# Performance work log

Measured on AMD Instinct MI355X. Metric: run time of the kernel, lower is better.

Reference implementation:

```python
import jax, jax.numpy as jnp
import numpy as np

N_NODES = 50000
N_EDGES = 50000  # hyperedges
NNZ = 500000
N_GRAPHS = 50
IN_C, HID, OUT_C = 128, 256, 2


def _inv_deg(idx, num_segments):
    deg = jax.ops.segment_sum(jnp.ones(idx.shape[0], jnp.float32), idx, num_segments=num_segments)
    return jnp.where(deg > 0, 1.0 / deg, 0.0)


def hg_conv(x, W, b, rows, cols, dinv, binv):
    # PyG HypergraphConv (no attention, unit edge weights):
    # X' = D^{-1} H B^{-1} H^T (X Theta) + bias
    x = x @ W                                                    # [N, hid]
    e = jax.ops.segment_sum(x[rows], cols, num_segments=N_EDGES) * binv[:, None]   # edge feats [E, hid]
    out = jax.ops.segment_sum(e[cols], rows, num_segments=N_NODES) * dinv[:, None]  # node feats [N, hid]
    return out + b


def setup_inputs() -> dict:
    key = jax.random.key(0)
    ks = jax.random.split(key, 12)
    x = jax.random.normal(ks[0], (N_NODES, IN_C), jnp.float32)
    edge_index = jax.random.randint(ks[1], (2, NNZ), 0, N_EDGES, dtype=jnp.int64)
    batch = jnp.sort(jax.random.randint(ks[2], (N_NODES,), 0, N_GRAPHS, dtype=jnp.int64))
    s = 0.05
    return {
        "x": x, "edge_index": edge_index, "batch": batch,
        "W0": jax.random.normal(ks[3], (IN_C, HID), jnp.float32) * s,
        "b0": jnp.zeros((HID,), jnp.float32),
        "W1": jax.random.normal(ks[4], (HID, HID), jnp.float32) * s,
        "b1": jnp.zeros((HID,), jnp.float32),
        "W2": jax.random.normal(ks[5], (HID, HID), jnp.float32) * s,
        "b2": jnp.zeros((HID,), jnp.float32),
        "M1": jax.random.normal(ks[6], (HID, HID), jnp.float32) * s,
        "bM1": jnp.zeros((HID,), jnp.float32),
        "M2": jax.random.normal(ks[7], (HID, OUT_C), jnp.float32) * s,
        "bM2": jnp.zeros((OUT_C,), jnp.float32),
    }


def reference(x, edge_index, batch, W0, b0, W1, b1, W2, b2, M1, bM1, M2, bM2):
    rows, cols = edge_index[0], edge_index[1]
    dinv = _inv_deg(rows, N_NODES)   # node degree inverse
    binv = _inv_deg(cols, N_EDGES)   # hyperedge degree inverse
    h = jax.nn.relu(hg_conv(x, W0, b0, rows, cols, dinv, binv))
    h = jax.nn.relu(hg_conv(h, W1, b1, rows, cols, dinv, binv))
    h = jax.nn.relu(hg_conv(h, W2, b2, rows, cols, dinv, binv))
    # global_mean_pool (dropout is identity in eval mode)
    cnt = jax.ops.segment_sum(jnp.ones(N_NODES, jnp.float32), batch, num_segments=N_GRAPHS)
    pooled = jax.ops.segment_sum(h, batch, num_segments=N_GRAPHS) / jnp.maximum(cnt, 1.0)[:, None]
    # MLP head
    out = jax.nn.relu(pooled @ M1 + bM1) @ M2 + bM2
    return out
```

## Files before the change

### kernel.cpp

```cpp
#include <hip/hip_runtime.h>
#include <hip/hip_bf16.h>

#define NN   50000
#define NE   50000
#define NNZV 500000
#define NG   50
#define INC  128
#define HID  256
#define OUTC 2
#define STRIDE 32

typedef __bf16 bf16_t;
typedef __bf16 bf16x8 __attribute__((ext_vector_type(8)));
typedef float  f32x4  __attribute__((ext_vector_type(4)));
typedef float  f32x2  __attribute__((ext_vector_type(2)));

__device__ __forceinline__ bf16_t f2b(float f) {
  union { __hip_bfloat16 h; bf16_t b; } u;
  u.h = __float2bfloat16(f);
  return u.b;
}
__device__ __forceinline__ float b2f(bf16_t b) { return (float)b; }

template <bool HI>
__device__ __forceinline__ unsigned int fp8_pk2(float a, float b, unsigned int old) {
  return __builtin_amdgcn_cvt_pk_fp8_f32(a, b, old, HI);
}
__device__ __forceinline__ uint4 fp8_pk16(const float* v) {
  uint4 o;
  unsigned int* ow = &o.x;
#pragma unroll
  for (int wd = 0; wd < 4; wd++) {
    unsigned int u = fp8_pk2<false>(v[wd * 4 + 0], v[wd * 4 + 1], 0u);
    ow[wd] = fp8_pk2<true>(v[wd * 4 + 2], v[wd * 4 + 3], u);
  }
  return o;
}
__device__ __forceinline__ void fp8_acc16(uint4 v, f32x2* a2) {
  a2[0] += __builtin_amdgcn_cvt_pk_f32_fp8(v.x, false);
  a2[1] += __builtin_amdgcn_cvt_pk_f32_fp8(v.x, true);
  a2[2] += __builtin_amdgcn_cvt_pk_f32_fp8(v.y, false);
  a2[3] += __builtin_amdgcn_cvt_pk_f32_fp8(v.y, true);
  a2[4] += __builtin_amdgcn_cvt_pk_f32_fp8(v.z, false);
  a2[5] += __builtin_amdgcn_cvt_pk_f32_fp8(v.z, true);
  a2[6] += __builtin_amdgcn_cvt_pk_f32_fp8(v.w, false);
  a2[7] += __builtin_amdgcn_cvt_pk_f32_fp8(v.w, true);
}

__device__ __forceinline__ void wswiz_one(const float* __restrict__ W, bf16_t* __restrict__ wsw, int t) {
  int lane = t & 63;
  int nt   = (t >> 6) & 15;
  int kc   = t >> 10;
  int q = lane >> 4, n16 = lane & 15;
  bf16x8 o;
#pragma unroll
  for (int j = 0; j < 8; j++)
    o[j] = f2b(W[(size_t)(kc * 32 + q * 8 + j) * HID + nt * 16 + n16]);
  reinterpret_cast<bf16x8*>(wsw)[t] = o;
}

#define FILL_EPT   4
#define FILL_CHUNK (256 * FILL_EPT)
#define FILL_B     ((NNZV + FILL_CHUNK - 1) / FILL_CHUNK)
#define PREP_BX 1563
#define PREP_BW 80
#define PREP_BG 196

__global__ void build_kernel(const int* __restrict__ rows, const int* __restrict__ cols,
                             int* __restrict__ ncur, int* __restrict__ ecur,
                             unsigned short* __restrict__ ncol, unsigned short* __restrict__ erow,
                             const float* __restrict__ x, unsigned char* __restrict__ xb8,
                             const float* __restrict__ W0, const float* __restrict__ W1,
                             const float* __restrict__ W2, bf16_t* __restrict__ w0,
                             bf16_t* __restrict__ w1, bf16_t* __restrict__ w2,
                             const int* __restrict__ batch, int* __restrict__ gstart) {
  int blk = blockIdx.x;
  if (blk < 2 * FILL_B) {
    const bool nodeside = blk >= FILL_B;
    int local = nodeside ? blk - FILL_B : blk;
    int base  = local * FILL_CHUNK + threadIdx.x;
    int key[FILL_EPT], val[FILL_EPT], slot[FILL_EPT];
    bool ok[FILL_EPT];
#pragma unroll
    for (int e = 0; e < FILL_EPT; e++) {
      int i  = base + e * 256;
      ok[e]  = (i < NNZV);
      int ii = ok[e] ? i : 0;
      int r = rows[ii], c = cols[ii];
      key[e] = nodeside ? r : c;
      val[e] = nodeside ? c : r;
    }
    int* cur             = nodeside ? ncur : ecur;
    unsigned short* lstd = nodeside ? ncol : erow;
#pragma unroll
    for (int e = 0; e < FILL_EPT; e++)
      if (ok[e]) slot[e] = atomicAdd(&cur[key[e]], 1);
#pragma unroll
    for (int e = 0; e < FILL_EPT; e++)
      if (ok[e] && slot[e] < STRIDE)
        lstd[((size_t)key[e] << 5) + slot[e]] = (unsigned short)val[e];
  } else if (blk < 2 * FILL_B + PREP_BX) {
    int t = (blk - 2 * FILL_B) * 256 + threadIdx.x;
    if (t >= NN * INC / 16) return;
    const f32x4* p = reinterpret_cast<const f32x4*>(x) + (size_t)t * 4;
    float v[16];
#pragma unroll
    for (int wd = 0; wd < 4; wd++) {
      f32x4 q4 = p[wd];
#pragma unroll
      for (int j = 0; j < 4; j++) v[wd * 4 + j] = q4[j];
    }
    reinterpret_cast<uint4*>(xb8)[t] = fp8_pk16(v);
  } else if (blk < 2 * FILL_B + PREP_BX + PREP_BW) {
    int t = (blk - 2 * FILL_B - PREP_BX) * 256 + threadIdx.x;
    const int C0 = (INC / 32) * 1024;
    const int C1 = (HID / 32) * 1024;
    if (t < C0)                wswiz_one(W0, w0, t);
    else if (t < C0 + C1)      wswiz_one(W1, w1, t - C0);
    else if (t < C0 + 2 * C1)  wswiz_one(W2, w2, t - C0 - C1);
  } else {
    int i = (blk - 2 * FILL_B - PREP_BX - PREP_BW) * 256 + threadIdx.x;
    if (i >= NN) return;
    int cur  = batch[i];
    int prev = (i == 0) ? -1 : batch[i - 1];
    for (int g = prev + 1; g <= cur; g++) gstart[g] = i;
    if (i == NN - 1) {
      for (int g = cur + 1; g <= NG; g++) gstart[g] = NN;
    }
  }
}

template <int K>
__device__ __forceinline__ void gather_direct(const unsigned char* __restrict__ src,
                                              const int* __restrict__ cnt,
                                              const unsigned short* __restrict__ lst,
                                              int seg, int lr, float* acc, int& c) {
  constexpr int LPR = K / 16;
  c = min(cnt[seg], STRIDE);
  const unsigned short* p = lst + ((size_t)seg << 5);
  const uint4* sv = reinterpret_cast<const uint4*>(src);
  f32x2* a2 = reinterpret_cast<f32x2*>(acc);
#pragma unroll
  for (int k = 0; k < 8; k++) a2[k] = f32x2{0.f, 0.f};
  for (int i0 = 0; i0 < c; i0 += 8) {
    int m = c - i0;
    uint4 v[8];
#pragma unroll
    for (int j = 0; j < 8; j++)
      if (j < m) v[j] = sv[(size_t)p[i0 + j] * LPR + lr];
#pragma unroll
    for (int j = 0; j < 8; j++)
      if (j < m) fp8_acc16(v[j], a2);
  }
}

template <int W>
__global__ __launch_bounds__(256) void seg_gather_kernel(const unsigned char* __restrict__ src,
                                                         const int* __restrict__ cnt,
                                                         const unsigned short* __restrict__ lst,
                                                         unsigned char* __restrict__ dst, int nseg) {
  constexpr int LPR = W / 16;
  constexpr int SPW = 64 / LPR;
  constexpr int SPB = 4 * SPW;
  const int lane = threadIdx.x & 63;
  const int wid  = threadIdx.x >> 6;
  const int sub  = lane / LPR, lr = lane % LPR;
  int seg = blockIdx.x * SPB + wid * SPW + sub;
  if (seg >= nseg) return;
  float acc[16];
  int c;
  gather_direct<W>(src, cnt, lst, seg, lr, acc, c);
  float sc = (c > 0) ? (1.0f / (float)c) : 0.f;
  float v16[16];
#pragma unroll
  for (int k = 0; k < 16; k++) v16[k] = acc[k] * sc;
  reinterpret_cast<uint4*>(dst + (size_t)seg * W + lr * 16)[0] = fp8_pk16(v16);
}

template <int K, bool GRELU, bool EPI, bool OUT8>
__global__ __launch_bounds__(256) void ngemm_kernel(const unsigned char* __restrict__ src,
                                                    const int* __restrict__ cnt,
                                                    const unsigned short* __restrict__ lst,
                                                    const float* __restrict__ gbias,
                                                    const bf16_t* __restrict__ wsw,
                                                    const float* __restrict__ ebias,
                                                    void* __restrict__ Bout, int M) {
  constexpr int SW = K + 8;
  __shared__ bf16_t arows[16 * SW];
  const int tid  = threadIdx.x;
  const int wid  = tid >> 6;
  const int lane = tid & 63;
  const int mblk = blockIdx.x * 16;

  constexpr int LPR = K / 16;
  constexpr int SPW = 64 / LPR;
  const int sub = lane / LPR, lr = lane % LPR;
  {
    int row = wid * SPW + sub;
    int seg = mblk + row;
    if (seg < M) {
      float acc[16];
      int c;
      gather_direct<K>(src, cnt, lst, seg, lr, acc, c);
      float sc = (c > 0) ? (1.0f / (float)c) : 0.f;
      bf16_t* dp = arows + row * SW + lr * 16;
      bf16x8 o0, o1;
#pragma unroll
      for (int k = 0; k < 8; k++) {
        float v0 = acc[k] * sc, v1 = acc[k + 8] * sc;
        if constexpr (GRELU) {
          v0 = fmaxf(v0 + gbias[lr * 16 + k], 0.f);
          v1 = fmaxf(v1 + gbias[lr * 16 + k + 8], 0.f);
        }
        o0[k] = f2b(v0);
        o1[k] = f2b(v1);
      }
      reinterpret_cast<bf16x8*>(dp)[0] = o0;
      reinterpret_cast<bf16x8*>(dp)[1] = o1;
    }
  }
  __syncthreads();

  const int q = lane >> 4, n16 = lane & 15;
  f32x4 acc2[4];
#pragma unroll
  for (int j = 0; j < 4; j++) acc2[j] = f32x4{0.f, 0.f, 0.f, 0.f};

  const bf16x8* wv = reinterpret_cast<const bf16x8*>(wsw);
  for (int kc = 0; kc < K / 32; kc++) {
    bf16x8 af = *reinterpret_cast<const bf16x8*>(arows + n16 * SW + kc * 32 + q * 8);
    const bf16x8* wp = wv + (size_t)kc * 1024 + (size_t)(wid * 4) * 64 + lane;
#pragma unroll
    for (int j = 0; j < 4; j++) {
      bf16x8 bf = wp[j * 64];
      acc2[j] = __builtin_amdgcn_mfma_f32_16x16x32_bf16(af, bf, acc2[j], 0, 0, 0);
    }
  }

  float bcol[4];
  if constexpr (EPI) {
#pragma unroll
    for (int j = 0; j < 4; j++) bcol[j] = ebias[(wid * 4 + j) * 16 + n16];
  }

  int mb = mblk + q * 4;
#pragma unroll
  for (int r = 0; r < 4; r++) {
    int m = mb + r;
    if (m < M) {
      if constexpr (OUT8) {
        unsigned char* dst = (unsigned char*)Bout + (size_t)m * HID + n16;
#pragma unroll
        for (int j = 0; j < 4; j++) {
          float v = acc2[j][r];
          if constexpr (EPI) v = fmaxf(v + bcol[j], 0.f);
          unsigned int wbits = fp8_pk2<false>(v, v, 0u);
          dst[(wid * 4 + j) << 4] = (unsigned char)(wbits & 0xffu);
        }
      } else {
        bf16_t* dst = (bf16_t*)Bout + (size_t)m * HID + n16;
#pragma unroll
        for (int j = 0; j < 4; j++) {
          float v = acc2[j][r];
          if constexpr (EPI) v = fmaxf(v + bcol[j], 0.f);
          dst[(wid * 4 + j) << 4] = f2b(v);
        }
      }
    }
  }
}

template <int K>
__global__ __launch_bounds__(256) void ngemm2_kernel(const unsigned char* __restrict__ src,
                                                     const int* __restrict__ cnt,
                                                     const unsigned short* __restrict__ lst,
                                                     const bf16_t* __restrict__ wswA,
                                                     const float* __restrict__ biasA,
                                                     const bf16_t* __restrict__ wswB,
                                                     unsigned char* __restrict__ Bout, int M) {
  constexpr int SW  = K + 8;
  constexpr int SW2 = HID + 8;
  constexpr int LPR = K / 16;
  constexpr int SPW = 64 / LPR;
  __shared__ bf16_t arows[32 * SW];
  __shared__ bf16_t brows[32 * SW2];
  const int tid  = threadIdx.x;
  const int wid  = tid >> 6;
  const int lane = tid & 63;
  const int mblk = blockIdx.x * 32;

  {
    const int sub = lane / LPR, lr = lane % LPR;
    int row = wid * SPW + sub;
    int seg = mblk + row;
    if (seg < M) {
      float acc[16];
      int c;
      gather_direct<K>(src, cnt, lst, seg, lr, acc, c);
      float sc = (c > 0) ? (1.0f / (float)c) : 0.f;
      bf16_t* dp = arows + row * SW + lr * 16;
      bf16x8 o0, o1;
#pragma unroll
      for (int k = 0; k < 8; k++) {
        o0[k] = f2b(acc[k] * sc);
        o1[k] = f2b(acc[k + 8] * sc);
      }
      reinterpret_cast<bf16x8*>(dp)[0] = o0;
      reinterpret_cast<bf16x8*>(dp)[1] = o1;
    }
  }
  __syncthreads();

  const int q = lane >> 4, n16 = lane & 15;
  {
    f32x4 acc2[2][4];
#pragma unroll
    for (int a = 0; a < 2; a++)
#pragma unroll
      for (int j = 0; j < 4; j++) acc2[a][j] = f32x4{0.f, 0.f, 0.f, 0.f};
    const bf16x8* wv = reinterpret_cast<const bf16x8*>(wswA);
    for (int kc = 0; kc < K / 32; kc++) {
      bf16x8 af0 = *reinterpret_cast<const bf16x8*>(arows + n16 * SW + kc * 32 + q * 8);
      bf16x8 af1 = *reinterpret_cast<const bf16x8*>(arows + (n16 + 16) * SW + kc * 32 + q * 8);
      const bf16x8* wp = wv + (size_t)kc * 1024 + (size_t)(wid * 4) * 64 + lane;
#pragma unroll
      for (int j = 0; j < 4; j++) {
        bf16x8 bf = wp[j * 64];
        acc2[0][j] = __builtin_amdgcn_mfma_f32_16x16x32_bf16(af0, bf, acc2[0][j], 0, 0, 0);
        acc2[1][j] = __builtin_amdgcn_mfma_f32_16x16x32_bf16(af1, bf, acc2[1][j], 0, 0, 0);
      }
    }
#pragma unroll
    for (int a = 0; a < 2; a++) {
#pragma unroll
      for (int j = 0; j < 4; j++) {
        float bj = biasA[(wid * 4 + j) * 16 + n16];
#pragma unroll
        for (int r = 0; r < 4; r++) {
          float v = fmaxf(acc2[a][j][r] + bj, 0.f);
          brows[(a * 16 + q * 4 + r) * SW2 + (wid * 4 + j) * 16 + n16] = f2b(v);
        }
      }
    }
  }
  __syncthreads();

  f32x4 acc3[2][4];
#pragma unroll
  for (int a = 0; a < 2; a++)
#pragma unroll
    for (int j = 0; j < 4; j++) acc3[a][j] = f32x4{0.f, 0.f, 0.f, 0.f};
  const bf16x8* wv = reinterpret_cast<const bf16x8*>(wswB);
  for (int kc = 0; kc < HID / 32; kc++) {
    bf16x8 af0 = *reinterpret_cast<const bf16x8*>(brows + n16 * SW2 + kc * 32 + q * 8);
    bf16x8 af1 = *reinterpret_cast<const bf16x8*>(brows + (n16 + 16) * SW2 + kc * 32 + q * 8);
    const bf16x8* wp = wv + (size_t)kc * 1024 + (size_t)(wid * 4) * 64 + lane;
#pragma unroll
    for (int j = 0; j < 4; j++) {
      bf16x8 bf = wp[j * 64];
      acc3[0][j] = __builtin_amdgcn_mfma_f32_16x16x32_bf16(af0, bf, acc3[0][j], 0, 0, 0);
      acc3[1][j] = __builtin_amdgcn_mfma_f32_16x16x32_bf16(af1, bf, acc3[1][j], 0, 0, 0);
    }
  }

#pragma unroll
  for (int a = 0; a < 2; a++) {
    int mb = mblk + a * 16 + q * 4;
#pragma unroll
    for (int r = 0; r < 4; r++) {
      int m = mb + r;
      if (m < M) {
        unsigned char* dst = Bout + (size_t)m * HID + n16;
#pragma unroll
        for (int j = 0; j < 4; j++) {
          float v = acc3[a][j][r];
          unsigned int wbits = fp8_pk2<false>(v, v, 0u);
          dst[(wid * 4 + j) << 4] = (unsigned char)(wbits & 0xffu);
        }
      }
    }
  }
}

__global__ __launch_bounds__(256) void npool_kernel(const unsigned char* __restrict__ src,
                                                    const int* __restrict__ cnt,
                                                    const unsigned short* __restrict__ lst,
                                                    const float* __restrict__ bias,
                                                    const int* __restrict__ batch,
                                                    float* __restrict__ pooled) {
  constexpr int K = HID, SW = K + 8;
  __shared__ bf16_t arows[16 * SW];
  const int tid  = threadIdx.x;
  const int wid  = tid >> 6;
  const int lane = tid & 63;
  const int mblk = blockIdx.x * 16;

  constexpr int LPR = K / 16;
  constexpr int SPW = 64 / LPR;
  const int sub = lane / LPR, lr = lane % LPR;
  {
    int row = wid * SPW + sub;
    int seg = mblk + row;
    if (seg < NN) {
      float acc[16];
      int c;
      gather_direct<K>(src, cnt, lst, seg, lr, acc, c);
      float sc = (c > 0) ? (1.0f / (float)c) : 0.f;
      bf16_t* dp = arows + row * SW + lr * 16;
      bf16x8 o0, o1;
#pragma unroll
      for (int k = 0; k < 8; k++) {
        o0[k] = f2b(fmaxf(acc[k] * sc + bias[lr * 16 + k], 0.f));
        o1[k] = f2b(fmaxf(acc[k + 8] * sc + bias[lr * 16 + k + 8], 0.f));
      }
      reinterpret_cast<bf16x8*>(dp)[0] = o0;
      reinterpret_cast<bf16x8*>(dp)[1] = o1;
    }
  }
  __syncthreads();

  int f = tid;
  float acc = 0.f;
  int curg = -1;
  for (int r = 0; r < 16; r++) {
    int node = mblk + r;
    if (node >= NN) break;
    int g = batch[node];
    if (g != curg) {
      if (curg >= 0) atomicAdd(&pooled[(size_t)curg * HID + f], acc);
      curg = g; acc = 0.f;
    }
    acc += b2f(arows[r * SW + f]);
  }
  if (curg >= 0) atomicAdd(&pooled[(size_t)curg * HID + f], acc);
}

__global__ void head_kernel(const float* __restrict__ pooled, const int* __restrict__ gstart,
                            const float* __restrict__ M1, const float* __restrict__ bM1,
                            const float* __restrict__ M2, const float* __restrict__ bM2,
                            float* __restrict__ out) {
  int g = blockIdx.x;
  int t = threadIdx.x;
  __shared__ float p[HID];
  __shared__ float red[256];
  float cntf = (float)(gstart[g + 1] - gstart[g]);
  float inv = 1.f / fmaxf(cntf, 1.f);
  p[t] = pooled[(size_t)g * HID + t] * inv;
  __syncthreads();
  float h = bM1[t];
  for (int k = 0; k < HID; k++) h += p[k] * M1[k * HID + t];
  h = fmaxf(h, 0.f);
  float c0 = h * M2[t * OUTC + 0];
  float c1 = h * M2[t * OUTC + 1];
  red[t] = c0;
  __syncthreads();
  for (int off = 128; off > 0; off >>= 1) {
    if (t < off) red[t] += red[t + off];
    __syncthreads();
  }
  float s0 = 0.f;
  if (t == 0) s0 = red[0];
  __syncthreads();
  red[t] = c1;
  __syncthreads();
  for (int off = 128; off > 0; off >>= 1) {
    if (t < off) red[t] += red[t + off];
    __syncthreads();
  }
  if (t == 0) {
    out[g * 2 + 0] = s0 + bM2[0];
    out[g * 2 + 1] = red[0] + bM2[1];
  }
}

extern "C" void kernel_launch(void* const* d_in, const int* in_sizes, int n_in,
                              void* d_out, int out_size, void* d_ws, size_t ws_size,
                              hipStream_t stream) {
  const float* x   = (const float*)d_in[0];
  const int* ei    = (const int*)d_in[1];
  const int* rows  = ei;
  const int* cols  = ei + NNZV;
  const int* batch = (const int*)d_in[2];
  const float* W0  = (const float*)d_in[3];
  const float* b0  = (const float*)d_in[4];
  const float* W1  = (const float*)d_in[5];
  const float* b1  = (const float*)d_in[6];
  const float* W2  = (const float*)d_in[7];
  const float* b2  = (const float*)d_in[8];
  const float* M1  = (const float*)d_in[9];
  const float* bM1 = (const float*)d_in[10];
  const float* M2  = (const float*)d_in[11];
  const float* bM2 = (const float*)d_in[12];
  float* out       = (float*)d_out;

  char* w = (char*)d_ws;
  size_t off = 0;
  bf16_t* P = (bf16_t*)(w + off); off += (size_t)NN * HID * 2;
  bf16_t* Q = (bf16_t*)(w + off); off += (size_t)NE * HID * 2;
  bf16_t* R = (bf16_t*)(w + off); off += (size_t)NN * HID * 2;
  bf16_t* wsw0 = (bf16_t*)(w + off); off += (size_t)INC * HID * 2;
  bf16_t* wsw1 = (bf16_t*)(w + off); off += (size_t)HID * HID * 2;
  bf16_t* wsw2 = (bf16_t*)(w + off); off += (size_t)HID * HID * 2;
  int* gstart   = (int*)(w + off);   off += (size_t)(NG + 1) * 4;
  size_t zoff = off;
  float* pooled = (float*)(w + off); off += (size_t)NG * HID * 4;
  int* ncur     = (int*)(w + off);   off += (size_t)NN * 4;
  int* ecur     = (int*)(w + off);   off += (size_t)NE * 4;
  size_t zbytes = off - zoff;
  off = (off + 63) & ~(size_t)63;
  unsigned short* erow = (unsigned short*)(w + off); off += (size_t)NE * STRIDE * 2;
  unsigned short* ncol = (unsigned short*)(w + off); off += (size_t)NN * STRIDE * 2;

  unsigned char* xb8 = (unsigned char*)R;
  unsigned char* Qe8 = (unsigned char*)Q;
  unsigned char* Q8  = (unsigned char*)Q;
  unsigned char* P8  = (unsigned char*)P;

  (void)hipMemsetAsync(w + zoff, 0, zbytes, stream);

  const int BN = 256;
  build_kernel<<<2 * FILL_B + PREP_BX + PREP_BW + PREP_BG, BN, 0, stream>>>(
      rows, cols, ncur, ecur, ncol, erow, x, xb8, W0, W1, W2, wsw0, wsw1, wsw2, batch, gstart);

  seg_gather_kernel<INC><<<(NE + 31) / 32, BN, 0, stream>>>(xb8, ecur, erow, Qe8, NE);
  ngemm2_kernel<INC><<<(NN + 31) / 32, BN, 0, stream>>>(Qe8, ncur, ncol, wsw0, b0, wsw1, P8, NN);
  seg_gather_kernel<HID><<<(NE + 15) / 16, BN, 0, stream>>>(P8, ecur, erow, Q8, NE);
  ngemm_kernel<HID, true, false, true><<<(NN + 15) / 16, BN, 0, stream>>>(
      Q8, ncur, ncol, b1, wsw2, nullptr, P8, NN);
  seg_gather_kernel<HID><<<(NE + 15) / 16, BN, 0, stream>>>(P8, ecur, erow, Q8, NE);
  npool_kernel<<<(NN + 15) / 16, BN, 0, stream>>>(Q8, ncur, ncol, b2, batch, pooled);

  head_kernel<<<NG, 256, 0, stream>>>(pooled, gstart, M1, bM1, M2, bM2, out);
}
```

Baseline: 335.8 us.

## Overlap node-side CSR fill and weight prep with first edge gather; unroll gather

The build kernel now fills only the edge-side adjacency and converts x to fp8. The node-side adjacency fill, weight swizzle and graph-start computation move into a new kernel that also runs the first edge gather, so independent work shares one launch and the old standalone gather launch disappears. Separately, gather_direct now loads each segment's 32-entry index list with four vector loads and runs a fixed, software-pipelined unrolled schedule of up to 32 neighbours with double-buffered loads, in place of the variable loop over scalar index reads. The fixed unroll raises register pressure and issues predicated code even for low-degree segments.

New measurement: 353.3 us. +5.2%, slower.

```diff
diff --git a/kernel.cpp b/kernel.cpp
--- a/kernel.cpp
+++ b/kernel.cpp
@@ -66,41 +66,37 @@
 #define PREP_BW 80
 #define PREP_BG 196
 
+__device__ __forceinline__ void fill_side(const int* __restrict__ keys, const int* __restrict__ vals,
+                                          int* __restrict__ cur, unsigned short* __restrict__ lstd,
+                                          int local) {
+  int base = local * FILL_CHUNK + threadIdx.x;
+  int key[FILL_EPT], val[FILL_EPT], slot[FILL_EPT];
+  bool ok[FILL_EPT];
+#pragma unroll
+  for (int e = 0; e < FILL_EPT; e++) {
+    int i  = base + e * 256;
+    ok[e]  = (i < NNZV);
+    int ii = ok[e] ? i : 0;
+    key[e] = keys[ii];
+    val[e] = vals[ii];
+  }
+#pragma unroll
+  for (int e = 0; e < FILL_EPT; e++)
+    if (ok[e]) slot[e] = atomicAdd(&cur[key[e]], 1);
+#pragma unroll
+  for (int e = 0; e < FILL_EPT; e++)
+    if (ok[e] && slot[e] < STRIDE)
+      lstd[((size_t)key[e] << 5) + slot[e]] = (unsigned short)val[e];
+}
+
 __global__ void build_kernel(const int* __restrict__ rows, const int* __restrict__ cols,
-                             int* __restrict__ ncur, int* __restrict__ ecur,
-                             unsigned short* __restrict__ ncol, unsigned short* __restrict__ erow,
-                             const float* __restrict__ x, unsigned char* __restrict__ xb8,
-                             const float* __restrict__ W0, const float* __restrict__ W1,
-                             const float* __restrict__ W2, bf16_t* __restrict__ w0,
-                             bf16_t* __restrict__ w1, bf16_t* __restrict__ w2,
-                             const int* __restrict__ batch, int* __restrict__ gstart) {
+                             int* __restrict__ ecur, unsigned short* __restrict__ erow,
+                             const float* __restrict__ x, unsigned char* __restrict__ xb8) {
   int blk = blockIdx.x;
-  if (blk < 2 * FILL_B) {
-    const bool nodeside = blk >= FILL_B;
-    int local = nodeside ? blk - FILL_B : blk;
-    int base  = local * FILL_CHUNK + threadIdx.x;
-    int key[FILL_EPT], val[FILL_EPT], slot[FILL_EPT];
-    bool ok[FILL_EPT];
-#pragma unroll
-    for (int e = 0; e < FILL_EPT; e++) {
-      int i  = base + e * 256;
-      ok[e]  = (i < NNZV);
-      int ii = ok[e] ? i : 0;
-      int r = rows[ii], c = cols[ii];
-      key[e] = nodeside ? r : c;
-      val[e] = nodeside ? c : r;
-    }
-    int* cur             = nodeside ? ncur : ecur;
-    unsigned short* lstd = nodeside ? ncol : erow;
-#pragma unroll
-    for (int e = 0; e < FILL_EPT; e++)
-      if (ok[e]) slot[e] = atomicAdd(&cur[key[e]], 1);
-#pragma unroll
-    for (int e = 0; e < FILL_EPT; e++)
-      if (ok[e] && slot[e] < STRIDE)
-        lstd[((size_t)key[e] << 5) + slot[e]] = (unsigned short)val[e];
-  } else if (blk < 2 * FILL_B + PREP_BX) {
-    int t = (blk - 2 * FILL_B) * 256 + threadIdx.x;
+  if (blk < FILL_B) {
+    fill_side(cols, rows, ecur, erow, blk);
+  } else {
+    int t = (blk - FILL_B) * 256 + threadIdx.x;
     if (t >= NN * INC / 16) return;
     const f32x4* p = reinterpret_cast<const f32x4*>(x) + (size_t)t * 4;
     float v[16];
@@ -111,22 +107,6 @@
       for (int j = 0; j < 4; j++) v[wd * 4 + j] = q4[j];
     }
     reinterpret_cast<uint4*>(xb8)[t] = fp8_pk16(v);
-  } else if (blk < 2 * FILL_B + PREP_BX + PREP_BW) {
-    int t = (blk - 2 * FILL_B - PREP_BX) * 256 + threadIdx.x;
-    const int C0 = (INC / 32) * 1024;
-    const int C1 = (HID / 32) * 1024;
-    if (t < C0)                wswiz_one(W0, w0, t);
-    else if (t < C0 + C1)      wswiz_one(W1, w1, t - C0);
-    else if (t < C0 + 2 * C1)  wswiz_one(W2, w2, t - C0 - C1);
-  } else {
-    int i = (blk - 2 * FILL_B - PREP_BX - PREP_BW) * 256 + threadIdx.x;
-    if (i >= NN) return;
-    int cur  = batch[i];
-    int prev = (i == 0) ? -1 : batch[i - 1];
-    for (int g = prev + 1; g <= cur; g++) gstart[g] = i;
-    if (i == NN - 1) {
-      for (int g = cur + 1; g <= NG; g++) gstart[g] = NN;
-    }
   }
 }
 
@@ -137,21 +117,33 @@
                                               int seg, int lr, float* acc, int& c) {
   constexpr int LPR = K / 16;
   c = min(cnt[seg], STRIDE);
-  const unsigned short* p = lst + ((size_t)seg << 5);
+  const uint4* lp = reinterpret_cast<const uint4*>(lst + ((size_t)seg << 5));
+  uint4 la = lp[0], lb = lp[1], lc4 = lp[2], ld = lp[3];
+  unsigned int lw[16] = {la.x, la.y, la.z, la.w, lb.x, lb.y, lb.z, lb.w,
+                         lc4.x, lc4.y, lc4.z, lc4.w, ld.x, ld.y, ld.z, ld.w};
   const uint4* sv = reinterpret_cast<const uint4*>(src);
   f32x2* a2 = reinterpret_cast<f32x2*>(acc);
 #pragma unroll
   for (int k = 0; k < 8; k++) a2[k] = f32x2{0.f, 0.f};
-  for (int i0 = 0; i0 < c; i0 += 8) {
-    int m = c - i0;
-    uint4 v[8];
-#pragma unroll
-    for (int j = 0; j < 8; j++)
-      if (j < m) v[j] = sv[(size_t)p[i0 + j] * LPR + lr];
-#pragma unroll
-    for (int j = 0; j < 8; j++)
-      if (j < m) fp8_acc16(v[j], a2);
-  }
+  uint4 v0[8], v1[8];
+#define GADDR(j) ((size_t)((lw[(j) >> 1] >> (((j) & 1) * 16)) & 0xffffu) * LPR + lr)
+#pragma unroll
+  for (int j = 0; j < 8; j++) if (j < c) v0[j] = sv[GADDR(j)];
+#pragma unroll
+  for (int j = 0; j < 8; j++) if (8 + j < c) v1[j] = sv[GADDR(8 + j)];
+#pragma unroll
+  for (int j = 0; j < 8; j++) if (j < c) fp8_acc16(v0[j], a2);
+#pragma unroll
+  for (int j = 0; j < 8; j++) if (16 + j < c) v0[j] = sv[GADDR(16 + j)];
+#pragma unroll
+  for (int j = 0; j < 8; j++) if (8 + j < c) fp8_acc16(v1[j], a2);
+#pragma unroll
+  for (int j = 0; j < 8; j++) if (24 + j < c) v1[j] = sv[GADDR(24 + j)];
+#pragma unroll
+  for (int j = 0; j < 8; j++) if (16 + j < c) fp8_acc16(v0[j], a2);
+#pragma unroll
+  for (int j = 0; j < 8; j++) if (24 + j < c) fp8_acc16(v1[j], a2);
+#undef GADDR
 }
 
 template <int W>
@@ -175,6 +167,61 @@
 #pragma unroll
   for (int k = 0; k < 16; k++) v16[k] = acc[k] * sc;
   reinterpret_cast<uint4*>(dst + (size_t)seg * W + lr * 16)[0] = fp8_pk16(v16);
+}
+
+#define E0_G ((NE + 31) / 32)
+
+__global__ __launch_bounds__(256) void e0_kernel(const unsigned char* __restrict__ xb8,
+                                                 const int* __restrict__ ecur,
+                                                 const unsigned short* __restrict__ erow,
+                                                 unsigned char* __restrict__ dst,
+                                                 const int* __restrict__ rows,
+                                                 const int* __restrict__ cols,
+                                                 int* __restrict__ ncur,
+                                                 unsigned short* __restrict__ ncol,
+                                                 const float* __restrict__ W0,
+                                                 const float* __restrict__ W1,
+                                                 const float* __restrict__ W2,
+                                                 bf16_t* __restrict__ w0, bf16_t* __restrict__ w1,
+                                                 bf16_t* __restrict__ w2,
+                                                 const int* __restrict__ batch,
+                                                 int* __restrict__ gstart) {
+  int blk = blockIdx.x;
+  if (blk < E0_G) {
+    constexpr int LPR = INC / 16;
+    constexpr int SPW = 64 / LPR;
+    const int lane = threadIdx.x & 63;
+    const int wid  = threadIdx.x >> 6;
+    const int sub  = lane / LPR, lr = lane % LPR;
+    int seg = blk * 32 + wid * SPW + sub;
+    if (seg >= NE) return;
+    float acc[16];
+    int c;
+    gather_direct<INC>(xb8, ecur, erow, seg, lr, acc, c);
+    float sc = (c > 0) ? (1.0f / (float)c) : 0.f;
+    float v16[16];
+#pragma unroll
+    for (int k = 0; k < 16; k++) v16[k] = acc[k] * sc;
+    reinterpret_cast<uint4*>(dst + (size_t)seg * INC + lr * 16)[0] = fp8_pk16(v16);
+  } else if (blk < E0_G + FILL_B) {
+    fill_side(rows, cols, ncur, ncol, blk - E0_G);
+  } else if (blk < E0_G + FILL_B + PREP_BW) {
+    int t = (blk - E0_G - FILL_B) * 256 + threadIdx.x;
+    const int C0 = (INC / 32) * 1024;
+    const int C1 = (HID / 32) * 1024;
+    if (t < C0)                wswiz_one(W0, w0, t);
+    else if (t < C0 + C1)      wswiz_one(W1, w1, t - C0);
+    else if (t < C0 + 2 * C1)  wswiz_one(W2, w2, t - C0 - C1);
+  } else {
+    int i = (blk - E0_G - FILL_B - PREP_BW) * 256 + threadIdx.x;
+    if (i >= NN) return;
+    int cur  = batch[i];
+    int prev = (i == 0) ? -1 : batch[i - 1];
+    for (int g = prev + 1; g <= cur; g++) gstart[g] = i;
+    if (i == NN - 1) {
+      for (int g = cur + 1; g <= NG; g++) gstart[g] = NN;
+    }
+  }
 }
 
 template <int K, bool GRELU, bool EPI, bool OUT8>
@@ -519,10 +566,11 @@
   (void)hipMemsetAsync(w + zoff, 0, zbytes, stream);
 
   const int BN = 256;
-  build_kernel<<<2 * FILL_B + PREP_BX + PREP_BW + PREP_BG, BN, 0, stream>>>(
-      rows, cols, ncur, ecur, ncol, erow, x, xb8, W0, W1, W2, wsw0, wsw1, wsw2, batch, gstart);
-
-  seg_gather_kernel<INC><<<(NE + 31) / 32, BN, 0, stream>>>(xb8, ecur, erow, Qe8, NE);
+  build_kernel<<<FILL_B + PREP_BX, BN, 0, stream>>>(rows, cols, ecur, erow, x, xb8);
+
+  e0_kernel<<<E0_G + FILL_B + PREP_BW + PREP_BG, BN, 0, stream>>>(
+      xb8, ecur, erow, Qe8, rows, cols, ncur, ncol, W0, W1, W2, wsw0, wsw1, wsw2, batch, gstart);
+
   ngemm2_kernel<INC><<<(NN + 31) / 32, BN, 0, stream>>>(Qe8, ncur, ncol, wsw0, b0, wsw1, P8, NN);
   seg_gather_kernel<HID><<<(NE + 15) / 16, BN, 0, stream>>>(P8, ecur, erow, Q8, NE);
   ngemm_kernel<HID, true, false, true><<<(NN + 15) / 16, BN, 0, stream>>>(
```

## Split fused gather+GEMM into feature-sliced gather kernels and standalone GEMMs

Applied to the files above, without the earlier changes.

Unfuses the node-side gather from the MFMA GEMM kernels. Gathering now runs in a new feature-sliced kernel where each block handles one of 8 column slices, the 32-entry neighbor list is loaded up front, and loads are software-pipelined in two batches of 8. Results go to bf16 intermediates that separate GEMM kernels read. Pooling changes from per-tile atomics to a per-graph reduction using gstart. This targets gather latency and occupancy, traded against extra launches and an extra bf16 round-trip through memory for the node features.

Result: slower. 526.2 us (+56.7%).

```diff
diff --git a/kernel.cpp b/kernel.cpp
--- a/kernel.cpp
+++ b/kernel.cpp
@@ -65,6 +65,29 @@
 #define PREP_BX 1563
 #define PREP_BW 80
 #define PREP_BG 196
+
+__device__ __forceinline__ void fill_side(const int* __restrict__ keys, const int* __restrict__ vals,
+                                          int* __restrict__ cur, unsigned short* __restrict__ lstd,
+                                          int local) {
+  int base = local * FILL_CHUNK + threadIdx.x;
+  int key[FILL_EPT], val[FILL_EPT], slot[FILL_EPT];
+  bool ok[FILL_EPT];
+#pragma unroll
+  for (int e = 0; e < FILL_EPT; e++) {
+    int i  = base + e * 256;
+    ok[e]  = (i < NNZV);
+    int ii = ok[e] ? i : 0;
+    key[e] = keys[ii];
+    val[e] = vals[ii];
+  }
+#pragma unroll
+  for (int e = 0; e < FILL_EPT; e++)
+    if (ok[e]) slot[e] = atomicAdd(&cur[key[e]], 1);
+#pragma unroll
+  for (int e = 0; e < FILL_EPT; e++)
+    if (ok[e] && slot[e] < STRIDE)
+      lstd[((size_t)key[e] << 5) + slot[e]] = (unsigned short)val[e];
+}
 
 __global__ void build_kernel(const int* __restrict__ rows, const int* __restrict__ cols,
                              int* __restrict__ ncur, int* __restrict__ ecur,
@@ -76,29 +99,8 @@
                              const int* __restrict__ batch, int* __restrict__ gstart) {
   int blk = blockIdx.x;
   if (blk < 2 * FILL_B) {
-    const bool nodeside = blk >= FILL_B;
-    int local = nodeside ? blk - FILL_B : blk;
-    int base  = local * FILL_CHUNK + threadIdx.x;
-    int key[FILL_EPT], val[FILL_EPT], slot[FILL_EPT];
-    bool ok[FILL_EPT];
-#pragma unroll
-    for (int e = 0; e < FILL_EPT; e++) {
-      int i  = base + e * 256;
-      ok[e]  = (i < NNZV);
-      int ii = ok[e] ? i : 0;
-      int r = rows[ii], c = cols[ii];
-      key[e] = nodeside ? r : c;
-      val[e] = nodeside ? c : r;
-    }
-    int* cur             = nodeside ? ncur : ecur;
-    unsigned short* lstd = nodeside ? ncol : erow;
-#pragma unroll
-    for (int e = 0; e < FILL_EPT; e++)
-      if (ok[e]) slot[e] = atomicAdd(&cur[key[e]], 1);
-#pragma unroll
-    for (int e = 0; e < FILL_EPT; e++)
-      if (ok[e] && slot[e] < STRIDE)
-        lstd[((size_t)key[e] << 5) + slot[e]] = (unsigned short)val[e];
+    if (blk < FILL_B) fill_side(cols, rows, ecur, erow, blk);
+    else              fill_side(rows, cols, ncur, ncol, blk - FILL_B);
   } else if (blk < 2 * FILL_B + PREP_BX) {
     int t = (blk - 2 * FILL_B) * 256 + threadIdx.x;
     if (t >= NN * INC / 16) return;
@@ -130,158 +132,80 @@
   }
 }
 
-template <int K>
-__device__ __forceinline__ void gather_direct(const unsigned char* __restrict__ src,
-                                              const int* __restrict__ cnt,
-                                              const unsigned short* __restrict__ lst,
-                                              int seg, int lr, float* acc, int& c) {
-  constexpr int LPR = K / 16;
-  c = min(cnt[seg], STRIDE);
-  const unsigned short* p = lst + ((size_t)seg << 5);
-  const uint4* sv = reinterpret_cast<const uint4*>(src);
+template <int K, bool OUT8, bool BR>
+__global__ __launch_bounds__(256) void sgath_kernel(const unsigned char* __restrict__ src,
+                                                    const int* __restrict__ cnt,
+                                                    const unsigned short* __restrict__ lst,
+                                                    const float* __restrict__ bias,
+                                                    void* __restrict__ dst, int nseg) {
+  constexpr int SLB  = K / 8;
+  constexpr int LS   = SLB / 16;
+  constexpr int SPB  = 256 / LS;
+  constexpr int RSTR = K / 16;
+  const int slice = blockIdx.x & 7;
+  const int tile  = blockIdx.x >> 3;
+  const int t     = threadIdx.x;
+  const int seg   = tile * SPB + t / LS;
+  const int lr    = t % LS;
+  if (seg >= nseg) return;
+  const int fo = slice * SLB + lr * 16;
+  int c = min(cnt[seg], STRIDE);
+  const uint4* lp = reinterpret_cast<const uint4*>(lst + ((size_t)seg << 5));
+  uint4 la = lp[0], lb = lp[1], lc4 = lp[2], ld = lp[3];
+  unsigned int lw[16] = {la.x, la.y, la.z, la.w, lb.x, lb.y, lb.z, lb.w,
+                         lc4.x, lc4.y, lc4.z, lc4.w, ld.x, ld.y, ld.z, ld.w};
+  const uint4* sv = reinterpret_cast<const uint4*>(src) + (fo >> 4);
+  float acc[16];
   f32x2* a2 = reinterpret_cast<f32x2*>(acc);
 #pragma unroll
   for (int k = 0; k < 8; k++) a2[k] = f32x2{0.f, 0.f};
-  for (int i0 = 0; i0 < c; i0 += 8) {
-    int m = c - i0;
-    uint4 v[8];
-#pragma unroll
-    for (int j = 0; j < 8; j++)
-      if (j < m) v[j] = sv[(size_t)p[i0 + j] * LPR + lr];
-#pragma unroll
-    for (int j = 0; j < 8; j++)
-      if (j < m) fp8_acc16(v[j], a2);
-  }
-}
-
-template <int W>
-__global__ __launch_bounds__(256) void seg_gather_kernel(const unsigned char* __restrict__ src,
-                                                         const int* __restrict__ cnt,
-                                                         const unsigned short* __restrict__ lst,
-                                                         unsigned char* __restrict__ dst, int nseg) {
-  constexpr int LPR = W / 16;
-  constexpr int SPW = 64 / LPR;
-  constexpr int SPB = 4 * SPW;
-  const int lane = threadIdx.x & 63;
-  const int wid  = threadIdx.x >> 6;
-  const int sub  = lane / LPR, lr = lane % LPR;
-  int seg = blockIdx.x * SPB + wid * SPW + sub;
-  if (seg >= nseg) return;
-  float acc[16];
-  int c;
-  gather_direct<W>(src, cnt, lst, seg, lr, acc, c);
+  uint4 v0[8], v1[8];
+#define GADDR(j) ((size_t)((lw[(j) >> 1] >> (((j) & 1) * 16)) & 0xffffu) * RSTR)
+#pragma unroll
+  for (int j = 0; j < 8; j++) if (j < c) v0[j] = sv[GADDR(j)];
+#pragma unroll
+  for (int j = 0; j < 8; j++) if (8 + j < c) v1[j] = sv[GADDR(8 + j)];
+#pragma unroll
+  for (int j = 0; j < 8; j++) if (j < c) fp8_acc16(v0[j], a2);
+#pragma unroll
+  for (int j = 0; j < 8; j++) if (16 + j < c) v0[j] = sv[GADDR(16 + j)];
+#pragma unroll
+  for (int j = 0; j < 8; j++) if (8 + j < c) fp8_acc16(v1[j], a2);
+#pragma unroll
+  for (int j = 0; j < 8; j++) if (24 + j < c) v1[j] = sv[GADDR(24 + j)];
+#pragma unroll
+  for (int j = 0; j < 8; j++) if (16 + j < c) fp8_acc16(v0[j], a2);
+#pragma unroll
+  for (int j = 0; j < 8; j++) if (24 + j < c) fp8_acc16(v1[j], a2);
+#undef GADDR
   float sc = (c > 0) ? (1.0f / (float)c) : 0.f;
   float v16[16];
 #pragma unroll
-  for (int k = 0; k < 16; k++) v16[k] = acc[k] * sc;
-  reinterpret_cast<uint4*>(dst + (size_t)seg * W + lr * 16)[0] = fp8_pk16(v16);
-}
-
-template <int K, bool GRELU, bool EPI, bool OUT8>
-__global__ __launch_bounds__(256) void ngemm_kernel(const unsigned char* __restrict__ src,
-                                                    const int* __restrict__ cnt,
-                                                    const unsigned short* __restrict__ lst,
-                                                    const float* __restrict__ gbias,
-                                                    const bf16_t* __restrict__ wsw,
-                                                    const float* __restrict__ ebias,
-                                                    void* __restrict__ Bout, int M) {
-  constexpr int SW = K + 8;
-  __shared__ bf16_t arows[16 * SW];
-  const int tid  = threadIdx.x;
-  const int wid  = tid >> 6;
-  const int lane = tid & 63;
-  const int mblk = blockIdx.x * 16;
-
-  constexpr int LPR = K / 16;
-  constexpr int SPW = 64 / LPR;
-  const int sub = lane / LPR, lr = lane % LPR;
-  {
-    int row = wid * SPW + sub;
-    int seg = mblk + row;
-    if (seg < M) {
-      float acc[16];
-      int c;
-      gather_direct<K>(src, cnt, lst, seg, lr, acc, c);
-      float sc = (c > 0) ? (1.0f / (float)c) : 0.f;
-      bf16_t* dp = arows + row * SW + lr * 16;
-      bf16x8 o0, o1;
-#pragma unroll
-      for (int k = 0; k < 8; k++) {
-        float v0 = acc[k] * sc, v1 = acc[k + 8] * sc;
-        if constexpr (GRELU) {
-          v0 = fmaxf(v0 + gbias[lr * 16 + k], 0.f);
-          v1 = fmaxf(v1 + gbias[lr * 16 + k + 8], 0.f);
-        }
-        o0[k] = f2b(v0);
-        o1[k] = f2b(v1);
-      }
-      reinterpret_cast<bf16x8*>(dp)[0] = o0;
-      reinterpret_cast<bf16x8*>(dp)[1] = o1;
-    }
-  }
-  __syncthreads();
-
-  const int q = lane >> 4, n16 = lane & 15;
-  f32x4 acc2[4];
-#pragma unroll
-  for (int j = 0; j < 4; j++) acc2[j] = f32x4{0.f, 0.f, 0.f, 0.f};
-
-  const bf16x8* wv = reinterpret_cast<const bf16x8*>(wsw);
-  for (int kc = 0; kc < K / 32; kc++) {
-    bf16x8 af = *reinterpret_cast<const bf16x8*>(arows + n16 * SW + kc * 32 + q * 8);
-    const bf16x8* wp = wv + (size_t)kc * 1024 + (size_t)(wid * 4) * 64 + lane;
-#pragma unroll
-    for (int j = 0; j < 4; j++) {
-      bf16x8 bf = wp[j * 64];
-      acc2[j] = __builtin_amdgcn_mfma_f32_16x16x32_bf16(af, bf, acc2[j], 0, 0, 0);
-    }
-  }
-
-  float bcol[4];
-  if constexpr (EPI) {
-#pragma unroll
-    for (int j = 0; j < 4; j++) bcol[j] = ebias[(wid * 4 + j) * 16 + n16];
-  }
-
-  int mb = mblk + q * 4;
-#pragma unroll
-  for (int r = 0; r < 4; r++) {
-    int m = mb + r;
-    if (m < M) {
-      if constexpr (OUT8) {
-        unsigned char* dst = (unsigned char*)Bout + (size_t)m * HID + n16;
-#pragma unroll
-        for (int j = 0; j < 4; j++) {
-          float v = acc2[j][r];
-          if constexpr (EPI) v = fmaxf(v + bcol[j], 0.f);
-          unsigned int wbits = fp8_pk2<false>(v, v, 0u);
-          dst[(wid * 4 + j) << 4] = (unsigned char)(wbits & 0xffu);
-        }
-      } else {
-        bf16_t* dst = (bf16_t*)Bout + (size_t)m * HID + n16;
-#pragma unroll
-        for (int j = 0; j < 4; j++) {
-          float v = acc2[j][r];
-          if constexpr (EPI) v = fmaxf(v + bcol[j], 0.f);
-          dst[(wid * 4 + j) << 4] = f2b(v);
-        }
-      }
-    }
-  }
-}
-
-template <int K>
-__global__ __launch_bounds__(256) void ngemm2_kernel(const unsigned char* __restrict__ src,
-                                                     const int* __restrict__ cnt,
-                                                     const unsigned short* __restrict__ lst,
+  for (int k = 0; k < 16; k++) {
+    float v = acc[k] * sc;
+    if constexpr (BR) v = fmaxf(v + bias[fo + k], 0.f);
+    v16[k] = v;
+  }
+  if constexpr (OUT8) {
+    *reinterpret_cast<uint4*>((unsigned char*)dst + (size_t)seg * K + fo) = fp8_pk16(v16);
+  } else {
+    bf16_t* dp = (bf16_t*)dst + (size_t)seg * K + fo;
+    bf16x8 o0, o1;
+#pragma unroll
+    for (int k = 0; k < 8; k++) { o0[k] = f2b(v16[k]); o1[k] = f2b(v16[k + 8]); }
+    reinterpret_cast<bf16x8*>(dp)[0] = o0;
+    reinterpret_cast<bf16x8*>(dp)[1] = o1;
+  }
+}
+
+__global__ __launch_bounds__(256) void gemm01_kernel(const bf16_t* __restrict__ A,
                                                      const bf16_t* __restrict__ wswA,
                                                      const float* __restrict__ biasA,
                                                      const bf16_t* __restrict__ wswB,
                                                      unsigned char* __restrict__ Bout, int M) {
+  constexpr int K   = INC;
   constexpr int SW  = K + 8;
   constexpr int SW2 = HID + 8;
-  constexpr int LPR = K / 16;
-  constexpr int SPW = 64 / LPR;
   __shared__ bf16_t arows[32 * SW];
   __shared__ bf16_t brows[32 * SW2];
   const int tid  = threadIdx.x;
@@ -289,25 +213,13 @@
   const int lane = tid & 63;
   const int mblk = blockIdx.x * 32;
 
-  {
-    const int sub = lane / LPR, lr = lane % LPR;
-    int row = wid * SPW + sub;
-    int seg = mblk + row;
-    if (seg < M) {
-      float acc[16];
-      int c;
-      gather_direct<K>(src, cnt, lst, seg, lr, acc, c);
-      float sc = (c > 0) ? (1.0f / (float)c) : 0.f;
-      bf16_t* dp = arows + row * SW + lr * 16;
-      bf16x8 o0, o1;
-#pragma unroll
-      for (int k = 0; k < 8; k++) {
-        o0[k] = f2b(acc[k] * sc);
-        o1[k] = f2b(acc[k + 8] * sc);
-      }
-      reinterpret_cast<bf16x8*>(dp)[0] = o0;
-      reinterpret_cast<bf16x8*>(dp)[1] = o1;
-    }
+#pragma unroll
+  for (int i = 0; i < 2; i++) {
+    int idx = tid + i * 256;
+    int row = idx >> 4, u = idx & 15;
+    if (mblk + row < M)
+      *reinterpret_cast<uint4*>(arows + row * SW + u * 8) =
+          *reinterpret_cast<const uint4*>(A + (size_t)(mblk + row) * K + u * 8);
   }
   __syncthreads();
 
@@ -362,7 +274,6 @@
       acc3[1][j] = __builtin_amdgcn_mfma_f32_16x16x32_bf16(af1, bf, acc3[1][j], 0, 0, 0);
     }
   }
-
 #pragma unroll
   for (int a = 0; a < 2; a++) {
     int mb = mblk + a * 16 + q * 4;
@@ -382,57 +293,85 @@
   }
 }
 
-__global__ __launch_bounds__(256) void npool_kernel(const unsigned char* __restrict__ src,
-                                                    const int* __restrict__ cnt,
-                                                    const unsigned short* __restrict__ lst,
-                                                    const float* __restrict__ bias,
-                                                    const int* __restrict__ batch,
-                                                    float* __restrict__ pooled) {
-  constexpr int K = HID, SW = K + 8;
-  __shared__ bf16_t arows[16 * SW];
+__global__ __launch_bounds__(256) void gemm2_kernel(const bf16_t* __restrict__ A,
+                                                    const bf16_t* __restrict__ wsw,
+                                                    unsigned char* __restrict__ Bout, int M) {
+  constexpr int K  = HID;
+  constexpr int SW = K + 8;
+  __shared__ bf16_t arows[32 * SW];
   const int tid  = threadIdx.x;
   const int wid  = tid >> 6;
   const int lane = tid & 63;
-  const int mblk = blockIdx.x * 16;
-
-  constexpr int LPR = K / 16;
-  constexpr int SPW = 64 / LPR;
-  const int sub = lane / LPR, lr = lane % LPR;
-  {
-    int row = wid * SPW + sub;
-    int seg = mblk + row;
-    if (seg < NN) {
-      float acc[16];
-      int c;
-      gather_direct<K>(src, cnt, lst, seg, lr, acc, c);
-      float sc = (c > 0) ? (1.0f / (float)c) : 0.f;
-      bf16_t* dp = arows + row * SW + lr * 16;
-      bf16x8 o0, o1;
-#pragma unroll
-      for (int k = 0; k < 8; k++) {
-        o0[k] = f2b(fmaxf(acc[k] * sc + bias[lr * 16 + k], 0.f));
-        o1[k] = f2b(fmaxf(acc[k + 8] * sc + bias[lr * 16 + k + 8], 0.f));
+  const int mblk = blockIdx.x * 32;
+
+#pragma unroll
+  for (int i = 0; i < 4; i++) {
+    int idx = tid + i * 256;
+    int row = idx >> 5, u = idx & 31;
+    if (mblk + row < M)
+      *reinterpret_cast<uint4*>(arows + row * SW + u * 8) =
+          *reinterpret_cast<const uint4*>(A + (size_t)(mblk + row) * K + u * 8);
+  }
+  __syncthreads();
+
+  const int q = lane >> 4, n16 = lane & 15;
+  f32x4 acc[2][4];
+#pragma unroll
+  for (int a = 0; a < 2; a++)
+#pragma unroll
+    for (int j = 0; j < 4; j++) acc[a][j] = f32x4{0.f, 0.f, 0.f, 0.f};
+  const bf16x8* wv = reinterpret_cast<const bf16x8*>(wsw);
+  for (int kc = 0; kc < K / 32; kc++) {
+    bf16x8 af0 = *reinterpret_cast<const bf16x8*>(arows + n16 * SW + kc * 32 + q * 8);
+    bf16x8 af1 = *reinterpret_cast<const bf16x8*>(arows + (n16 + 16) * SW + kc * 32 + q * 8);
+    const bf16x8* wp = wv + (size_t)kc * 1024 + (size_t)(wid * 4) * 64 + lane;
+#pragma unroll
+    for (int j = 0; j < 4; j++) {
+      bf16x8 bf = wp[j * 64];
+      acc[0][j] = __builtin_amdgcn_mfma_f32_16x16x32_bf16(af0, bf, acc[0][j], 0, 0, 0);
+      acc[1][j] = __builtin_amdgcn_mfma_f32_16x16x32_bf16(af1, bf, acc[1][j], 0, 0, 0);
+    }
+  }
+#pragma unroll
+  for (int a = 0; a < 2; a++) {
+    int mb = mblk + a * 16 + q * 4;
+#pragma unroll
+    for (int r = 0; r < 4; r++) {
+      int m = mb + r;
+      if (m < M) {
+        unsigned char* dst = Bout + (size_t)m * HID + n16;
+#pragma unroll
+        for (int j = 0; j < 4; j++) {
+          float v = acc[a][j][r];
+          unsigned int wbits = fp8_pk2<false>(v, v, 0u);
+          dst[(wid * 4 + j) << 4] = (unsigned char)(wbits & 0xffu);
+        }
       }
-      reinterpret_cast<bf16x8*>(dp)[0] = o0;
-      reinterpret_cast<bf16x8*>(dp)[1] = o1;
-    }
-  }
-  __syncthreads();
-
-  int f = tid;
+    }
+  }
+}
+
+__global__ __launch_bounds__(256) void pool_kernel(const bf16_t* __restrict__ N2,
+                                                   const int* __restrict__ gstart,
+                                                   float* __restrict__ pooled) {
+  int g  = blockIdx.x >> 3;
+  int fb = blockIdx.x & 7;
+  int t  = threadIdx.x;
+  int f  = fb * 32 + (t & 31);
+  int np = t >> 5;
+  int s = gstart[g], e = gstart[g + 1];
   float acc = 0.f;
-  int curg = -1;
-  for (int r = 0; r < 16; r++) {
-    int node = mblk + r;
-    if (node >= NN) break;
-    int g = batch[node];
-    if (g != curg) {
-      if (curg >= 0) atomicAdd(&pooled[(size_t)curg * HID + f], acc);
-      curg = g; acc = 0.f;
-    }
-    acc += b2f(arows[r * SW + f]);
-  }
-  if (curg >= 0) atomicAdd(&pooled[(size_t)curg * HID + f], acc);
+  for (int n = s + np; n < e; n += 8)
+    acc += b2f(N2[(size_t)n * HID + f]);
+  __shared__ float red[8][32];
+  red[np][t & 31] = acc;
+  __syncthreads();
+  if (t < 32) {
+    float s2 = 0.f;
+#pragma unroll
+    for (int p = 0; p < 8; p++) s2 += red[p][t];
+    pooled[(size_t)g * HID + fb * 32 + t] = s2;
+  }
 }
 
 __global__ void head_kernel(const float* __restrict__ pooled, const int* __restrict__ gstart,
@@ -495,9 +434,9 @@
 
   char* w = (char*)d_ws;
   size_t off = 0;
-  bf16_t* P = (bf16_t*)(w + off); off += (size_t)NN * HID * 2;
-  bf16_t* Q = (bf16_t*)(w + off); off += (size_t)NE * HID * 2;
-  bf16_t* R = (bf16_t*)(w + off); off += (size_t)NN * HID * 2;
+  char* Preg = w + off; off += (size_t)NN * HID * 2;
+  char* Qreg = w + off; off += (size_t)NE * HID * 2;
+  char* Rreg = w + off; off += (size_t)NN * HID * 2;
   bf16_t* wsw0 = (bf16_t*)(w + off); off += (size_t)INC * HID * 2;
   bf16_t* wsw1 = (bf16_t*)(w + off); off += (size_t)HID * HID * 2;
   bf16_t* wsw2 = (bf16_t*)(w + off); off += (size_t)HID * HID * 2;
@@ -511,10 +450,13 @@
   unsigned short* erow = (unsigned short*)(w + off); off += (size_t)NE * STRIDE * 2;
   unsigned short* ncol = (unsigned short*)(w + off); off += (size_t)NN * STRIDE * 2;
 
-  unsigned char* xb8 = (unsigned char*)R;
-  unsigned char* Qe8 = (unsigned char*)Q;
-  unsigned char* Q8  = (unsigned char*)Q;
-  unsigned char* P8  = (unsigned char*)P;
+  unsigned char* xb8 = (unsigned char*)Rreg;
+  bf16_t* N0 = (bf16_t*)(Rreg + (size_t)NN * INC);
+  bf16_t* N1 = (bf16_t*)Rreg;
+  unsigned char* Qe8 = (unsigned char*)Qreg;
+  unsigned char* Q8  = (unsigned char*)Qreg;
+  unsigned char* P8  = (unsigned char*)Preg;
+  bf16_t* N2 = (bf16_t*)Preg;
 
   (void)hipMemsetAsync(w + zoff, 0, zbytes, stream);
 
@@ -522,13 +464,19 @@
   build_kernel<<<2 * FILL_B + PREP_BX + PREP_BW + PREP_BG, BN, 0, stream>>>(
       rows, cols, ncur, ecur, ncol, erow, x, xb8, W0, W1, W2, wsw0, wsw1, wsw2, batch, gstart);
 
-  seg_gather_kernel<INC><<<(NE + 31) / 32, BN, 0, stream>>>(xb8, ecur, erow, Qe8, NE);
-  ngemm2_kernel<INC><<<(NN + 31) / 32, BN, 0, stream>>>(Qe8, ncur, ncol, wsw0, b0, wsw1, P8, NN);
-  seg_gather_kernel<HID><<<(NE + 15) / 16, BN, 0, stream>>>(P8, ecur, erow, Q8, NE);
-  ngemm_kernel<HID, true, false, true><<<(NN + 15) / 16, BN, 0, stream>>>(
-      Q8, ncur, ncol, b1, wsw2, nullptr, P8, NN);
-  seg_gather_kernel<HID><<<(NE + 15) / 16, BN, 0, stream>>>(P8, ecur, erow, Q8, NE);
-  npool_kernel<<<(NN + 15) / 16, BN, 0, stream>>>(Q8, ncur, ncol, b2, batch, pooled);
+  const int SG128 = 8 * ((NE + 255) / 256);
+  const int SG256 = 8 * ((NE + 127) / 128);
+  const int GG    = (NN + 31) / 32;
+
+  sgath_kernel<INC, true,  false><<<SG128, BN, 0, stream>>>(xb8, ecur, erow, nullptr, Qe8, NE);
+  sgath_kernel<INC, false, false><<<SG128, BN, 0, stream>>>(Qe8, ncur, ncol, nullptr, N0, NN);
+  gemm01_kernel<<<GG, BN, 0, stream>>>(N0, wsw0, b0, wsw1, P8, NN);
+  sgath_kernel<HID, true,  false><<<SG256, BN, 0, stream>>>(P8, ecur, erow, nullptr, Q8, NE);
+  sgath_kernel<HID, false, true ><<<SG256, BN, 0, stream>>>(Q8, ncur, ncol, b1, N1, NN);
+  gemm2_kernel<<<GG, BN, 0, stream>>>(N1, wsw2, P8, NN);
+  sgath_kernel<HID, true,  false><<<SG256, BN, 0, stream>>>(P8, ecur, erow, nullptr, Q8, NE);
+  sgath_kernel<HID, false, true ><<<SG256, BN, 0, stream>>>(Q8, ncur, ncol, b2, N2, NN);
+  pool_kernel<<<NG * 8, BN, 0, stream>>>(N2, gstart, pooled);
 
   head_kernel<<<NG, 256, 0, stream>>>(pooled, gstart, M1, bM1, M2, bM2, out);
 }
```
